# Kernel optimization log

Hardware: AMD Instinct MI355X
Metric: run time of the kernel (lower is better)

The kernel has to match this reference:

```python
import jax, jax.numpy as jnp
import numpy as np

B, C, H, W = 2, 256, 64, 64
NUM_HEADS = 4
HEAD_DIM = C // NUM_HEADS
N = H * W


def setup_inputs() -> dict:
    key = jax.random.key(0)
    ks = jax.random.split(key, 10)
    x = jax.random.normal(ks[0], (B, C, H, W), dtype=jnp.float32)
    # mostly-True mask; diagonal forced True so every row has a valid key
    m = jax.random.uniform(ks[1], (B, N, N)) > 0.1
    spatial_mask = m | jnp.eye(N, dtype=bool)[None]
    s = 1.0 / np.sqrt(C)
    wq = jax.random.normal(ks[2], (C, C), dtype=jnp.float32) * s
    bq = jnp.zeros((C,), jnp.float32)
    wk = jax.random.normal(ks[3], (C, C), dtype=jnp.float32) * s
    bk = jnp.zeros((C,), jnp.float32)
    wv = jax.random.normal(ks[4], (C, C), dtype=jnp.float32) * s
    bv = jnp.zeros((C,), jnp.float32)
    # torch zero-inits out_proj; use random weights for a non-trivial baseline
    wo = jax.random.normal(ks[5], (C, C), dtype=jnp.float32) * s
    bo = jnp.zeros((C,), jnp.float32)
    return {"x": x, "spatial_mask": spatial_mask, "wq": wq, "bq": bq,
            "wk": wk, "bk": bk, "wv": wv, "bv": bv, "wo": wo, "bo": bo}


def reference(x, spatial_mask, wq, bq, wk, bk, wv, bv, wo, bo):
    b, c, h, w = x.shape
    n = h * w
    nh, hd = NUM_HEADS, HEAD_DIM
    scale = hd ** -0.5
    x_flat = x.reshape(b, c, n).transpose(0, 2, 1)           # [b, n, c]
    q = (x_flat @ wq.T + bq).reshape(b, n, nh, hd).transpose(0, 2, 1, 3)
    k = (x_flat @ wk.T + bk).reshape(b, n, nh, hd).transpose(0, 2, 1, 3)
    v = (x_flat @ wv.T + bv).reshape(b, n, nh, hd).transpose(0, 2, 1, 3)
    logits = jnp.einsum('bhqd,bhkd->bhqk', q, k) * scale      # [b, nh, n, n]
    logits = jnp.where(spatial_mask[:, None], logits, -jnp.inf)
    attn = jax.nn.softmax(logits, axis=-1)                    # dropout = identity (eval)
    out = jnp.einsum('bhqk,bhkd->bhqd', attn, v)              # [b, nh, n, hd]
    out = out.transpose(0, 2, 1, 3).reshape(b, n, c)
    out = out @ wo.T + bo
    return out.transpose(0, 2, 1).reshape(b, c, h, w)
```

## Files before the change

kernel.cpp:

```cpp
#include <hip/hip_runtime.h>
#include <math.h>

namespace {
constexpr int B_    = 2;
constexpr int C_    = 256;
constexpr int NHEAD = 4;
constexpr int HDIM  = 64;
constexpr int NTOK  = 4096;
constexpr float SCALE = 0.125f;
constexpr float LOG2E = 1.44269504f;
}

typedef _Float16 half8  __attribute__((ext_vector_type(8)));
typedef _Float16 half4  __attribute__((ext_vector_type(4)));
typedef __fp16   fp16x2 __attribute__((ext_vector_type(2)));
typedef float    floatx4 __attribute__((ext_vector_type(4)));

__global__ __launch_bounds__(256) void pack_mask(
    const unsigned int* __restrict__ m32, unsigned int* __restrict__ packed)
{
    int c0 = 0, c1 = 0, c2 = 0, c3 = 0;
    #pragma unroll
    for (int i = 0; i < 16; i++) {
        const unsigned int d = m32[i];
        c0 += (d == 0x00000001u);
        c1 += (d == 0x3F803F80u);
        c2 += (d == 0x3F800000u);
        c3 += (d == 0x01010101u);
    }
    int fmt = 1, best = c1;
    if (c0 > best) { best = c0; fmt = 0; }
    if (c2 > best) { best = c2; fmt = 2; }
    if (c3 > best) { best = c3; fmt = 3; }

    const unsigned int W = blockIdx.x * 256 + threadIdx.x;
    unsigned int bits = 0;
    if (fmt == 1) {
        const uint4* p4 = (const uint4*)(m32 + (size_t)W * 16);
        #pragma unroll
        for (int i = 0; i < 4; i++) {
            const uint4 v = p4[i];
            const unsigned int d[4] = { v.x, v.y, v.z, v.w };
            #pragma unroll
            for (int j = 0; j < 4; j++) {
                const int e = i * 8 + j * 2;
                bits |= ((d[j] & 0xFFFFu) ? 1u : 0u) << e;
                bits |= ((d[j] >> 16)     ? 1u : 0u) << (e + 1);
            }
        }
    } else if (fmt != 3) {
        const uint4* p4 = (const uint4*)(m32 + (size_t)W * 32);
        #pragma unroll
        for (int i = 0; i < 8; i++) {
            const uint4 v = p4[i];
            bits |= (v.x ? 1u : 0u) << (i * 4 + 0);
            bits |= (v.y ? 1u : 0u) << (i * 4 + 1);
            bits |= (v.z ? 1u : 0u) << (i * 4 + 2);
            bits |= (v.w ? 1u : 0u) << (i * 4 + 3);
        }
    } else {
        const uint4* p4 = (const uint4*)(m32 + (size_t)W * 8);
        #pragma unroll
        for (int i = 0; i < 2; i++) {
            const uint4 v = p4[i];
            const unsigned int d[4] = { v.x, v.y, v.z, v.w };
            #pragma unroll
            for (int j = 0; j < 4; j++) {
                const int e = (i * 4 + j) * 4;
                bits |= ((d[j] & 0x000000FFu) ? 1u : 0u) << (e + 0);
                bits |= ((d[j] & 0x0000FF00u) ? 1u : 0u) << (e + 1);
                bits |= ((d[j] & 0x00FF0000u) ? 1u : 0u) << (e + 2);
                bits |= ((d[j] & 0xFF000000u) ? 1u : 0u) << (e + 3);
            }
        }
    }
    packed[W] = bits;
}

__global__ __launch_bounds__(256) void qkv_mfma(
    const float* __restrict__ x,
    const float* __restrict__ wq, const float* __restrict__ bq,
    const float* __restrict__ wk, const float* __restrict__ bk,
    const float* __restrict__ wv, const float* __restrict__ bv,
    _Float16* __restrict__ qo, _Float16* __restrict__ ko,
    _Float16* __restrict__ vo)
{
    const int nt = blockIdx.x;
    const int b  = blockIdx.y;
    const int p  = blockIdx.z;

    const float* w; const float* bias;
    if (p == 0)      { w = wq; bias = bq; }
    else if (p == 1) { w = wk; bias = bk; }
    else             { w = wv; bias = bv; }

    const int t    = threadIdx.x;
    const int wid  = t >> 6;
    const int lane = t & 63;
    const int quad = lane >> 4;
    const int l15  = lane & 15;
    const int n0   = nt * 64;

    __shared__ _Float16 xsh[64 * 264];
    __shared__ _Float16 wsh[64 * 72];
    __shared__ _Float16 tbuf[64 * 72];

    const int srow = t >> 2;
    const int sc   = (t & 3) * 16;

    {
        const int cr = t >> 4;
        const int nu = (t & 15) * 4;
        const float* xb = x + (size_t)b * C_ * NTOK;
        #pragma unroll
        for (int cc = 0; cc < 16; cc++) {
            const int cl = cc * 16 + cr;
            const float4 v = *(const float4*)&xb[(size_t)cl * NTOK + n0 + nu];
            xsh[(nu + 0) * 264 + cl] = (_Float16)v.x;
            xsh[(nu + 1) * 264 + cl] = (_Float16)v.y;
            xsh[(nu + 2) * 264 + cl] = (_Float16)v.z;
            xsh[(nu + 3) * 264 + cl] = (_Float16)v.w;
        }
    }

    for (int h = 0; h < NHEAD; h++) {
        const int co0 = h * 64;
        floatx4 acc[4];
        #pragma unroll
        for (int i = 0; i < 4; i++) acc[i] = (floatx4)0.f;

        for (int c0 = 0; c0 < C_; c0 += 64) {
            {
                const float* wr = &w[(size_t)(co0 + srow) * C_ + c0 + sc];
                half8 h0, h1;
                #pragma unroll
                for (int u = 0; u < 2; u++) {
                    const float4 a = *(const float4*)&wr[u * 4];
                    h0[u*4+0]=(_Float16)a.x; h0[u*4+1]=(_Float16)a.y;
                    h0[u*4+2]=(_Float16)a.z; h0[u*4+3]=(_Float16)a.w;
                }
                #pragma unroll
                for (int u = 0; u < 2; u++) {
                    const float4 a = *(const float4*)&wr[8 + u * 4];
                    h1[u*4+0]=(_Float16)a.x; h1[u*4+1]=(_Float16)a.y;
                    h1[u*4+2]=(_Float16)a.z; h1[u*4+3]=(_Float16)a.w;
                }
                *(half8*)&wsh[srow * 72 + sc]     = h0;
                *(half8*)&wsh[srow * 72 + sc + 8] = h1;
            }
            __syncthreads();
            const half8 a0 = *(const half8*)&wsh[(wid * 16 + l15) * 72 + quad * 8];
            const half8 a1 = *(const half8*)&wsh[(wid * 16 + l15) * 72 + 32 + quad * 8];
            #pragma unroll
            for (int nt2 = 0; nt2 < 4; nt2++) {
                const half8 b0 = *(const half8*)&xsh[(nt2 * 16 + l15) * 264 + c0 + quad * 8];
                const half8 b1 = *(const half8*)&xsh[(nt2 * 16 + l15) * 264 + c0 + 32 + quad * 8];
                acc[nt2] = __builtin_amdgcn_mfma_f32_16x16x32_f16(a0, b0, acc[nt2], 0, 0, 0);
                acc[nt2] = __builtin_amdgcn_mfma_f32_16x16x32_f16(a1, b1, acc[nt2], 0, 0, 0);
            }
            __syncthreads();
        }

        const float4 bb4 = *(const float4*)&bias[co0 + wid * 16 + quad * 4];
        const float bb[4] = { bb4.x, bb4.y, bb4.z, bb4.w };

        if (p < 2) {
            const float osc = (p == 0) ? (SCALE * LOG2E) : 1.0f;
            #pragma unroll
            for (int nt2 = 0; nt2 < 4; nt2++) {
                half4 hv;
                #pragma unroll
                for (int i = 0; i < 4; i++)
                    hv[i] = (_Float16)((acc[nt2][i] + bb[i]) * osc);
                *(half4*)&tbuf[(nt2 * 16 + l15) * 72 + wid * 16 + quad * 4] = hv;
            }
            __syncthreads();
            _Float16* dh = (p == 0 ? qo : ko) + (size_t)(b * NHEAD + h) * NTOK * HDIM;
            const half8 o0 = *(const half8*)&tbuf[srow * 72 + sc];
            const half8 o1 = *(const half8*)&tbuf[srow * 72 + sc + 8];
            *(half8*)&dh[(size_t)(n0 + srow) * HDIM + sc]     = o0;
            *(half8*)&dh[(size_t)(n0 + srow) * HDIM + sc + 8] = o1;
        } else {
            #pragma unroll
            for (int nt2 = 0; nt2 < 4; nt2++)
                #pragma unroll
                for (int i = 0; i < 4; i++)
                    tbuf[(wid * 16 + quad * 4 + i) * 72 + nt2 * 16 + l15] =
                        (_Float16)(acc[nt2][i] + bb[i]);
            __syncthreads();
            _Float16* vth = vo + (size_t)(b * NHEAD + h) * HDIM * NTOK;
            const half8 o0 = *(const half8*)&tbuf[srow * 72 + sc];
            const half8 o1 = *(const half8*)&tbuf[srow * 72 + sc + 8];
            *(half8*)&vth[(size_t)srow * NTOK + n0 + sc]     = o0;
            *(half8*)&vth[(size_t)srow * NTOK + n0 + sc + 8] = o1;
        }
        __syncthreads();
    }
}

__global__ __launch_bounds__(512) void attn(
    const _Float16* __restrict__ q, const _Float16* __restrict__ k,
    const _Float16* __restrict__ vt, const unsigned int* __restrict__ mpacked,
    _Float16* __restrict__ ao)
{
    const int b  = blockIdx.z;
    const int h  = blockIdx.y;
    const int q0 = blockIdx.x * 64;
    const int t    = threadIdx.x;
    const int w    = t >> 6;
    const int lane = t & 63;
    const int quad = lane >> 4;
    const int l15  = lane & 15;
    const int half = w >> 2;
    const int w4   = w & 3;
    const int koff = half * (NTOK / 2);

    __shared__ __align__(16) _Float16 ksA[64 * 72];
    __shared__ __align__(16) _Float16 vsA[64 * 72];
    __shared__ __align__(16) _Float16 psA[64 * 72];
    __shared__ __align__(16) _Float16 ksB[64 * 72];
    __shared__ __align__(16) _Float16 vsB[64 * 72];
    __shared__ __align__(16) _Float16 psB[64 * 72];

    _Float16* ksc = half ? ksB : ksA;
    _Float16* vsc = half ? vsB : vsA;
    _Float16* ps  = half ? psB : psA;

    const size_t head_off = (size_t)(b * NHEAD + h) * NTOK * HDIM;
    const _Float16* qb  = q  + head_off;
    const _Float16* kb  = k  + head_off;
    const _Float16* vtb = vt + head_off;
    const unsigned int* mrow = mpacked + (size_t)b * NTOK * 128;

    const int qrow = q0 + w4 * 16 + l15;
    half8 aq0 = *(const half8*)&qb[(size_t)qrow * HDIM + quad * 8];
    half8 aq1 = *(const half8*)&qb[(size_t)qrow * HDIM + 32 + quad * 8];
    const unsigned int* mq = &mrow[(size_t)qrow * 128];

    const int tl   = t & 255;
    const int srow = tl >> 2;
    const int scol = (tl & 3) * 16;

    half8 kreg0 = *(const half8*)&kb[(size_t)(koff + srow) * HDIM + scol];
    half8 kreg1 = *(const half8*)&kb[(size_t)(koff + srow) * HDIM + scol + 8];
    half8 vreg0 = *(const half8*)&vtb[(size_t)srow * NTOK + koff + scol];
    half8 vreg1 = *(const half8*)&vtb[(size_t)srow * NTOK + koff + scol + 8];

    float l_loc = 0.f;
    floatx4 o_acc[4];
    #pragma unroll
    for (int i = 0; i < 4; i++) o_acc[i] = (floatx4)0.f;

    _Float16* psrow = &ps[(w4 * 16 + l15) * 72];

    for (int kt = 0; kt < NTOK / 128; kt++) {
        const int k0 = koff + kt * 64;
        __syncthreads();
        *(half8*)&ksc[srow * 72 + scol]     = kreg0;
        *(half8*)&ksc[srow * 72 + scol + 8] = kreg1;
        *(half8*)&vsc[srow * 72 + scol]     = vreg0;
        *(half8*)&vsc[srow * 72 + scol + 8] = vreg1;
        __syncthreads();

        if (kt + 1 < NTOK / 128) {
            kreg0 = *(const half8*)&kb[(size_t)(k0 + 64 + srow) * HDIM + scol];
            kreg1 = *(const half8*)&kb[(size_t)(k0 + 64 + srow) * HDIM + scol + 8];
            vreg0 = *(const half8*)&vtb[(size_t)srow * NTOK + k0 + 64 + scol];
            vreg1 = *(const half8*)&vtb[(size_t)srow * NTOK + k0 + 64 + scol + 8];
        }
        const uint2 mw = *(const uint2*)&mq[k0 >> 5];

        floatx4 sa[4];
        #pragma unroll
        for (int ct = 0; ct < 4; ct++) {
            sa[ct] = (floatx4)0.f;
            const half8 ka0 = *(const half8*)&ksc[(ct * 16 + l15) * 72 + quad * 8];
            const half8 ka1 = *(const half8*)&ksc[(ct * 16 + l15) * 72 + 32 + quad * 8];
            sa[ct] = __builtin_amdgcn_mfma_f32_16x16x32_f16(ka0, aq0, sa[ct], 0, 0, 0);
            sa[ct] = __builtin_amdgcn_mfma_f32_16x16x32_f16(ka1, aq1, sa[ct], 0, 0, 0);
        }

        #pragma unroll
        for (int ct = 0; ct < 4; ct++) {
            const unsigned int word = (ct < 2) ? mw.x : mw.y;
            const unsigned nib = (word >> (((ct & 1) << 4) + quad * 4)) & 0xFu;
            const float p0 = __builtin_amdgcn_exp2f((nib & 1u) ? sa[ct][0] : -3.0e38f);
            const float p1 = __builtin_amdgcn_exp2f((nib & 2u) ? sa[ct][1] : -3.0e38f);
            const float p2 = __builtin_amdgcn_exp2f((nib & 4u) ? sa[ct][2] : -3.0e38f);
            const float p3 = __builtin_amdgcn_exp2f((nib & 8u) ? sa[ct][3] : -3.0e38f);
            l_loc += (p0 + p1) + (p2 + p3);
            const fp16x2 lo = __builtin_amdgcn_cvt_pkrtz(p0, p1);
            const fp16x2 hi = __builtin_amdgcn_cvt_pkrtz(p2, p3);
            half4 pv;
            pv[0] = (_Float16)lo[0]; pv[1] = (_Float16)lo[1];
            pv[2] = (_Float16)hi[0]; pv[3] = (_Float16)hi[1];
            *(half4*)&psrow[ct * 16 + quad * 4] = pv;
        }

        const half8 pb0 = *(const half8*)&psrow[quad * 8];
        const half8 pb1 = *(const half8*)&psrow[32 + quad * 8];
        #pragma unroll
        for (int dt = 0; dt < 4; dt++) {
            const half8 va0 = *(const half8*)&vsc[(dt * 16 + l15) * 72 + quad * 8];
            const half8 va1 = *(const half8*)&vsc[(dt * 16 + l15) * 72 + 32 + quad * 8];
            o_acc[dt] = __builtin_amdgcn_mfma_f32_16x16x32_f16(va0, pb0, o_acc[dt], 0, 0, 0);
            o_acc[dt] = __builtin_amdgcn_mfma_f32_16x16x32_f16(va1, pb1, o_acc[dt], 0, 0, 0);
        }
    }

    l_loc += __shfl_xor(l_loc, 16, 64);
    l_loc += __shfl_xor(l_loc, 32, 64);

    __syncthreads();
    float* oex = (float*)ksA;
    float* lex = (float*)vsA;
    if (w >= 4) {
        float* dst = &oex[((size_t)(w - 4) * 64 + lane) * 16];
        #pragma unroll
        for (int dt = 0; dt < 4; dt++)
            *(floatx4*)&dst[dt * 4] = o_acc[dt];
        if (quad == 0) lex[(w - 4) * 16 + l15] = l_loc;
    }
    __syncthreads();
    if (w < 4) {
        const float* src = &oex[((size_t)w * 64 + lane) * 16];
        const float lt = l_loc + lex[w * 16 + l15];
        const float inv = (lt > 0.f) ? (1.0f / lt) : 0.f;
        _Float16* aob = ao + ((size_t)b * NTOK + q0 + w * 16 + l15) * C_ + h * 64;
        #pragma unroll
        for (int dt = 0; dt < 4; dt++) {
            const floatx4 o2 = *(const floatx4*)&src[dt * 4];
            half4 r;
            #pragma unroll
            for (int rr = 0; rr < 4; rr++)
                r[rr] = (_Float16)((o_acc[dt][rr] + o2[rr]) * inv);
            *(half4*)&aob[dt * 16 + quad * 4] = r;
        }
    }
}

__global__ __launch_bounds__(256) void out_mfma(
    const _Float16* __restrict__ ao, const float* __restrict__ wo,
    const float* __restrict__ bo, float* __restrict__ out)
{
    const int nt  = blockIdx.x;
    const int cot = blockIdx.y;
    const int b   = blockIdx.z;
    const int t    = threadIdx.x;
    const int wid  = t >> 6;
    const int lane = t & 63;
    const int quad = lane >> 4;
    const int l15  = lane & 15;
    const int n0  = nt * 64;
    const int co0 = cot * 64;

    __shared__ _Float16 wsh[64 * 72];
    __shared__ _Float16 ash[64 * 72];
    __shared__ float    tf[64 * 68];

    const int srow = t >> 2;
    const int sc   = (t & 3) * 16;

    floatx4 acc[4];
    #pragma unroll
    for (int i = 0; i < 4; i++) acc[i] = (floatx4)0.f;

    const _Float16* aob = ao + ((size_t)b * NTOK + n0) * C_;

    for (int c0 = 0; c0 < C_; c0 += 64) {
        {
            const float* wr = &wo[(size_t)(co0 + srow) * C_ + c0 + sc];
            half8 h0, h1;
            #pragma unroll
            for (int u = 0; u < 2; u++) {
                const float4 a = *(const float4*)&wr[u * 4];
                h0[u*4+0]=(_Float16)a.x; h0[u*4+1]=(_Float16)a.y;
                h0[u*4+2]=(_Float16)a.z; h0[u*4+3]=(_Float16)a.w;
            }
            #pragma unroll
            for (int u = 0; u < 2; u++) {
                const float4 a = *(const float4*)&wr[8 + u * 4];
                h1[u*4+0]=(_Float16)a.x; h1[u*4+1]=(_Float16)a.y;
                h1[u*4+2]=(_Float16)a.z; h1[u*4+3]=(_Float16)a.w;
            }
            *(half8*)&wsh[srow * 72 + sc]     = h0;
            *(half8*)&wsh[srow * 72 + sc + 8] = h1;
        }
        {
            const _Float16* ar = &aob[(size_t)srow * C_ + c0 + sc];
            *(half8*)&ash[srow * 72 + sc]     = *(const half8*)&ar[0];
            *(half8*)&ash[srow * 72 + sc + 8] = *(const half8*)&ar[8];
        }
        __syncthreads();
        const half8 a0 = *(const half8*)&wsh[(wid * 16 + l15) * 72 + quad * 8];
        const half8 a1 = *(const half8*)&wsh[(wid * 16 + l15) * 72 + 32 + quad * 8];
        #pragma unroll
        for (int nt2 = 0; nt2 < 4; nt2++) {
            const half8 b0 = *(const half8*)&ash[(nt2 * 16 + l15) * 72 + quad * 8];
            const half8 b1 = *(const half8*)&ash[(nt2 * 16 + l15) * 72 + 32 + quad * 8];
            acc[nt2] = __builtin_amdgcn_mfma_f32_16x16x32_f16(a0, b0, acc[nt2], 0, 0, 0);
            acc[nt2] = __builtin_amdgcn_mfma_f32_16x16x32_f16(a1, b1, acc[nt2], 0, 0, 0);
        }
        __syncthreads();
    }

    #pragma unroll
    for (int nt2 = 0; nt2 < 4; nt2++)
        #pragma unroll
        for (int i = 0; i < 4; i++)
            tf[(wid * 16 + quad * 4 + i) * 68 + nt2 * 16 + l15] = acc[nt2][i];
    __syncthreads();

    const int row = t >> 2;
    const int c4  = (t & 3) * 16;
    const float bb = bo[co0 + row];
    float* orow = &out[((size_t)(b * C_ + co0 + row)) * NTOK + n0 + c4];
    #pragma unroll
    for (int u = 0; u < 4; u++) {
        float4 v = *(const float4*)&tf[row * 68 + c4 + u * 4];
        v.x += bb; v.y += bb; v.z += bb; v.w += bb;
        *(float4*)&orow[u * 4] = v;
    }
}

extern "C" void kernel_launch(void* const* d_in, const int* in_sizes, int n_in,
                              void* d_out, int out_size, void* d_ws, size_t ws_size,
                              hipStream_t stream) {
    const float* x    = (const float*)d_in[0];
    const void*  mask = d_in[1];
    const float* wq   = (const float*)d_in[2];
    const float* bq   = (const float*)d_in[3];
    const float* wk   = (const float*)d_in[4];
    const float* bk   = (const float*)d_in[5];
    const float* wv   = (const float*)d_in[6];
    const float* bv   = (const float*)d_in[7];
    const float* wo   = (const float*)d_in[8];
    const float* bo   = (const float*)d_in[9];
    float* out = (float*)d_out;

    const size_t qkv_elems = (size_t)B_ * NHEAD * NTOK * HDIM;
    _Float16* wsh = (_Float16*)d_ws;
    _Float16* qbuf  = wsh;
    _Float16* kbuf  = wsh + qkv_elems;
    _Float16* vtbuf = wsh + 2 * qkv_elems;
    _Float16* aobuf = wsh + 3 * qkv_elems;
    unsigned int* mpacked = (unsigned int*)(wsh + 4 * qkv_elems);

    pack_mask<<<dim3((B_ * NTOK * 128) / 256), 256, 0, stream>>>(
        (const unsigned int*)mask, mpacked);
    qkv_mfma<<<dim3(NTOK / 64, B_, 3), 256, 0, stream>>>(
        x, wq, bq, wk, bk, wv, bv, qbuf, kbuf, vtbuf);
    attn<<<dim3(NTOK / 64, NHEAD, B_), 512, 0, stream>>>(
        qbuf, kbuf, vtbuf, mpacked, aobuf);
    out_mfma<<<dim3(NTOK / 64, C_ / 64, B_), 256, 0, stream>>>(
        aobuf, wo, bo, out);
}
```

Baseline: 309.3 us.

## Split attention over four key ranges, merge partials in out-projection, fuse mask packing

The attention kernel now uses 256-thread blocks, each handling one quarter of the keys, with four times as many blocks. Unnormalized fp16 partial outputs and row sums are written to workspace. The output-projection kernel sums the four partials and normalizes them while staging its A tile. Mask packing moves into extra blocks of the QKV kernel, which removes one launch. The cost is four times the intermediate output traffic, partial sums accumulated in fp16, and the P tile now reusing the K shared buffer, which needs an extra barrier.

```diff
diff --git a/kernel.cpp b/kernel.cpp
--- a/kernel.cpp
+++ b/kernel.cpp
@@ -9,73 +9,13 @@
 constexpr int NTOK  = 4096;
 constexpr float SCALE = 0.125f;
 constexpr float LOG2E = 1.44269504f;
+constexpr int NSPLIT = 4;
 }
 
 typedef _Float16 half8  __attribute__((ext_vector_type(8)));
 typedef _Float16 half4  __attribute__((ext_vector_type(4)));
 typedef __fp16   fp16x2 __attribute__((ext_vector_type(2)));
 typedef float    floatx4 __attribute__((ext_vector_type(4)));
-
-__global__ __launch_bounds__(256) void pack_mask(
-    const unsigned int* __restrict__ m32, unsigned int* __restrict__ packed)
-{
-    int c0 = 0, c1 = 0, c2 = 0, c3 = 0;
-    #pragma unroll
-    for (int i = 0; i < 16; i++) {
-        const unsigned int d = m32[i];
-        c0 += (d == 0x00000001u);
-        c1 += (d == 0x3F803F80u);
-        c2 += (d == 0x3F800000u);
-        c3 += (d == 0x01010101u);
-    }
-    int fmt = 1, best = c1;
-    if (c0 > best) { best = c0; fmt = 0; }
-    if (c2 > best) { best = c2; fmt = 2; }
-    if (c3 > best) { best = c3; fmt = 3; }
-
-    const unsigned int W = blockIdx.x * 256 + threadIdx.x;
-    unsigned int bits = 0;
-    if (fmt == 1) {
-        const uint4* p4 = (const uint4*)(m32 + (size_t)W * 16);
-        #pragma unroll
-        for (int i = 0; i < 4; i++) {
-            const uint4 v = p4[i];
-            const unsigned int d[4] = { v.x, v.y, v.z, v.w };
-            #pragma unroll
-            for (int j = 0; j < 4; j++) {
-                const int e = i * 8 + j * 2;
-                bits |= ((d[j] & 0xFFFFu) ? 1u : 0u) << e;
-                bits |= ((d[j] >> 16)     ? 1u : 0u) << (e + 1);
-            }
-        }
-    } else if (fmt != 3) {
-        const uint4* p4 = (const uint4*)(m32 + (size_t)W * 32);
-        #pragma unroll
-        for (int i = 0; i < 8; i++) {
-            const uint4 v = p4[i];
-            bits |= (v.x ? 1u : 0u) << (i * 4 + 0);
-            bits |= (v.y ? 1u : 0u) << (i * 4 + 1);
-            bits |= (v.z ? 1u : 0u) << (i * 4 + 2);
-            bits |= (v.w ? 1u : 0u) << (i * 4 + 3);
-        }
-    } else {
-        const uint4* p4 = (const uint4*)(m32 + (size_t)W * 8);
-        #pragma unroll
-        for (int i = 0; i < 2; i++) {
-            const uint4 v = p4[i];
-            const unsigned int d[4] = { v.x, v.y, v.z, v.w };
-            #pragma unroll
-            for (int j = 0; j < 4; j++) {
-                const int e = (i * 4 + j) * 4;
-                bits |= ((d[j] & 0x000000FFu) ? 1u : 0u) << (e + 0);
-                bits |= ((d[j] & 0x0000FF00u) ? 1u : 0u) << (e + 1);
-                bits |= ((d[j] & 0x00FF0000u) ? 1u : 0u) << (e + 2);
-                bits |= ((d[j] & 0xFF000000u) ? 1u : 0u) << (e + 3);
-            }
-        }
-    }
-    packed[W] = bits;
-}
 
 __global__ __launch_bounds__(256) void qkv_mfma(
     const float* __restrict__ x,
@@ -83,18 +23,83 @@
     const float* __restrict__ wk, const float* __restrict__ bk,
     const float* __restrict__ wv, const float* __restrict__ bv,
     _Float16* __restrict__ qo, _Float16* __restrict__ ko,
-    _Float16* __restrict__ vo)
+    _Float16* __restrict__ vo,
+    const unsigned int* __restrict__ m32, unsigned int* __restrict__ packed)
 {
+    const int p = blockIdx.z;
+    const int t = threadIdx.x;
+
+    if (p == 3) {
+        int c0 = 0, c1 = 0, c2 = 0, c3 = 0;
+        #pragma unroll
+        for (int i = 0; i < 16; i++) {
+            const unsigned int d = m32[i];
+            c0 += (d == 0x00000001u);
+            c1 += (d == 0x3F803F80u);
+            c2 += (d == 0x3F800000u);
+            c3 += (d == 0x01010101u);
+        }
+        int fmt = 1, best = c1;
+        if (c0 > best) { best = c0; fmt = 0; }
+        if (c2 > best) { best = c2; fmt = 2; }
+        if (c3 > best) { best = c3; fmt = 3; }
+
+        const unsigned int pblk = blockIdx.y * 64 + blockIdx.x;
+        for (int it = 0; it < 32; it++) {
+            const unsigned int W = pblk * 8192 + it * 256 + t;
+            unsigned int bits = 0;
+            if (fmt == 1) {
+                const uint4* p4 = (const uint4*)(m32 + (size_t)W * 16);
+                #pragma unroll
+                for (int i = 0; i < 4; i++) {
+                    const uint4 v = p4[i];
+                    const unsigned int d[4] = { v.x, v.y, v.z, v.w };
+                    #pragma unroll
+                    for (int j = 0; j < 4; j++) {
+                        const int e = i * 8 + j * 2;
+                        bits |= ((d[j] & 0xFFFFu) ? 1u : 0u) << e;
+                        bits |= ((d[j] >> 16)     ? 1u : 0u) << (e + 1);
+                    }
+                }
+            } else if (fmt != 3) {
+                const uint4* p4 = (const uint4*)(m32 + (size_t)W * 32);
+                #pragma unroll
+                for (int i = 0; i < 8; i++) {
+                    const uint4 v = p4[i];
+                    bits |= (v.x ? 1u : 0u) << (i * 4 + 0);
+                    bits |= (v.y ? 1u : 0u) << (i * 4 + 1);
+                    bits |= (v.z ? 1u : 0u) << (i * 4 + 2);
+                    bits |= (v.w ? 1u : 0u) << (i * 4 + 3);
+                }
+            } else {
+                const uint4* p4 = (const uint4*)(m32 + (size_t)W * 8);
+                #pragma unroll
+                for (int i = 0; i < 2; i++) {
+                    const uint4 v = p4[i];
+                    const unsigned int d[4] = { v.x, v.y, v.z, v.w };
+                    #pragma unroll
+                    for (int j = 0; j < 4; j++) {
+                        const int e = (i * 4 + j) * 4;
+                        bits |= ((d[j] & 0x000000FFu) ? 1u : 0u) << (e + 0);
+                        bits |= ((d[j] & 0x0000FF00u) ? 1u : 0u) << (e + 1);
+                        bits |= ((d[j] & 0x00FF0000u) ? 1u : 0u) << (e + 2);
+                        bits |= ((d[j] & 0xFF000000u) ? 1u : 0u) << (e + 3);
+                    }
+                }
+            }
+            packed[W] = bits;
+        }
+        return;
+    }
+
     const int nt = blockIdx.x;
     const int b  = blockIdx.y;
-    const int p  = blockIdx.z;
 
     const float* w; const float* bias;
     if (p == 0)      { w = wq; bias = bq; }
     else if (p == 1) { w = wk; bias = bk; }
     else             { w = wv; bias = bv; }
 
-    const int t    = threadIdx.x;
     const int wid  = t >> 6;
     const int lane = t & 63;
     const int quad = lane >> 4;
@@ -198,33 +203,24 @@
     }
 }
 
-__global__ __launch_bounds__(512) void attn(
+__global__ __launch_bounds__(256, 8) void attn(
     const _Float16* __restrict__ q, const _Float16* __restrict__ k,
     const _Float16* __restrict__ vt, const unsigned int* __restrict__ mpacked,
-    _Float16* __restrict__ ao)
+    _Float16* __restrict__ aoP, float* __restrict__ lP)
 {
-    const int b  = blockIdx.z;
+    const int b  = blockIdx.z >> 2;
+    const int s  = blockIdx.z & 3;
     const int h  = blockIdx.y;
     const int q0 = blockIdx.x * 64;
     const int t    = threadIdx.x;
-    const int w    = t >> 6;
+    const int w4   = t >> 6;
     const int lane = t & 63;
     const int quad = lane >> 4;
     const int l15  = lane & 15;
-    const int half = w >> 2;
-    const int w4   = w & 3;
-    const int koff = half * (NTOK / 2);
-
-    __shared__ __align__(16) _Float16 ksA[64 * 72];
-    __shared__ __align__(16) _Float16 vsA[64 * 72];
-    __shared__ __align__(16) _Float16 psA[64 * 72];
-    __shared__ __align__(16) _Float16 ksB[64 * 72];
-    __shared__ __align__(16) _Float16 vsB[64 * 72];
-    __shared__ __align__(16) _Float16 psB[64 * 72];
-
-    _Float16* ksc = half ? ksB : ksA;
-    _Float16* vsc = half ? vsB : vsA;
-    _Float16* ps  = half ? psB : psA;
+    const int koff = s * (NTOK / NSPLIT);
+
+    __shared__ __align__(16) _Float16 ks[64 * 72];
+    __shared__ __align__(16) _Float16 vs[64 * 72];
 
     const size_t head_off = (size_t)(b * NHEAD + h) * NTOK * HDIM;
     const _Float16* qb  = q  + head_off;
@@ -237,9 +233,8 @@
     half8 aq1 = *(const half8*)&qb[(size_t)qrow * HDIM + 32 + quad * 8];
     const unsigned int* mq = &mrow[(size_t)qrow * 128];
 
-    const int tl   = t & 255;
-    const int srow = tl >> 2;
-    const int scol = (tl & 3) * 16;
+    const int srow = t >> 2;
+    const int scol = (t & 3) * 16;
 
     half8 kreg0 = *(const half8*)&kb[(size_t)(koff + srow) * HDIM + scol];
     half8 kreg1 = *(const half8*)&kb[(size_t)(koff + srow) * HDIM + scol + 8];
@@ -251,18 +246,18 @@
     #pragma unroll
     for (int i = 0; i < 4; i++) o_acc[i] = (floatx4)0.f;
 
-    _Float16* psrow = &ps[(w4 * 16 + l15) * 72];
-
-    for (int kt = 0; kt < NTOK / 128; kt++) {
+    _Float16* psrow = &ks[(w4 * 16 + l15) * 72];
+
+    for (int kt = 0; kt < NTOK / (64 * NSPLIT); kt++) {
         const int k0 = koff + kt * 64;
         __syncthreads();
-        *(half8*)&ksc[srow * 72 + scol]     = kreg0;
-        *(half8*)&ksc[srow * 72 + scol + 8] = kreg1;
-        *(half8*)&vsc[srow * 72 + scol]     = vreg0;
-        *(half8*)&vsc[srow * 72 + scol + 8] = vreg1;
-        __syncthreads();
-
-        if (kt + 1 < NTOK / 128) {
+        *(half8*)&ks[srow * 72 + scol]     = kreg0;
+        *(half8*)&ks[srow * 72 + scol + 8] = kreg1;
+        *(half8*)&vs[srow * 72 + scol]     = vreg0;
+        *(half8*)&vs[srow * 72 + scol + 8] = vreg1;
+        __syncthreads();
+
+        if (kt + 1 < NTOK / (64 * NSPLIT)) {
             kreg0 = *(const half8*)&kb[(size_t)(k0 + 64 + srow) * HDIM + scol];
             kreg1 = *(const half8*)&kb[(size_t)(k0 + 64 + srow) * HDIM + scol + 8];
             vreg0 = *(const half8*)&vtb[(size_t)srow * NTOK + k0 + 64 + scol];
@@ -274,11 +269,12 @@
         #pragma unroll
         for (int ct = 0; ct < 4; ct++) {
             sa[ct] = (floatx4)0.f;
-            const half8 ka0 = *(const half8*)&ksc[(ct * 16 + l15) * 72 + quad * 8];
-            const half8 ka1 = *(const half8*)&ksc[(ct * 16 + l15) * 72 + 32 + quad * 8];
+            const half8 ka0 = *(const half8*)&ks[(ct * 16 + l15) * 72 + quad * 8];
+            const half8 ka1 = *(const half8*)&ks[(ct * 16 + l15) * 72 + 32 + quad * 8];
             sa[ct] = __builtin_amdgcn_mfma_f32_16x16x32_f16(ka0, aq0, sa[ct], 0, 0, 0);
             sa[ct] = __builtin_amdgcn_mfma_f32_16x16x32_f16(ka1, aq1, sa[ct], 0, 0, 0);
         }
+        __syncthreads();
 
         #pragma unroll
         for (int ct = 0; ct < 4; ct++) {
@@ -301,8 +297,8 @@
         const half8 pb1 = *(const half8*)&psrow[32 + quad * 8];
         #pragma unroll
         for (int dt = 0; dt < 4; dt++) {
-            const half8 va0 = *(const half8*)&vsc[(dt * 16 + l15) * 72 + quad * 8];
-            const half8 va1 = *(const half8*)&vsc[(dt * 16 + l15) * 72 + 32 + quad * 8];
+            const half8 va0 = *(const half8*)&vs[(dt * 16 + l15) * 72 + quad * 8];
+            const half8 va1 = *(const half8*)&vs[(dt * 16 + l15) * 72 + 32 + quad * 8];
             o_acc[dt] = __builtin_amdgcn_mfma_f32_16x16x32_f16(va0, pb0, o_acc[dt], 0, 0, 0);
             o_acc[dt] = __builtin_amdgcn_mfma_f32_16x16x32_f16(va1, pb1, o_acc[dt], 0, 0, 0);
         }
@@ -311,37 +307,22 @@
     l_loc += __shfl_xor(l_loc, 16, 64);
     l_loc += __shfl_xor(l_loc, 32, 64);
 
-    __syncthreads();
-    float* oex = (float*)ksA;
-    float* lex = (float*)vsA;
-    if (w >= 4) {
-        float* dst = &oex[((size_t)(w - 4) * 64 + lane) * 16];
-        #pragma unroll
-        for (int dt = 0; dt < 4; dt++)
-            *(floatx4*)&dst[dt * 4] = o_acc[dt];
-        if (quad == 0) lex[(w - 4) * 16 + l15] = l_loc;
-    }
-    __syncthreads();
-    if (w < 4) {
-        const float* src = &oex[((size_t)w * 64 + lane) * 16];
-        const float lt = l_loc + lex[w * 16 + l15];
-        const float inv = (lt > 0.f) ? (1.0f / lt) : 0.f;
-        _Float16* aob = ao + ((size_t)b * NTOK + q0 + w * 16 + l15) * C_ + h * 64;
-        #pragma unroll
-        for (int dt = 0; dt < 4; dt++) {
-            const floatx4 o2 = *(const floatx4*)&src[dt * 4];
-            half4 r;
-            #pragma unroll
-            for (int rr = 0; rr < 4; rr++)
-                r[rr] = (_Float16)((o_acc[dt][rr] + o2[rr]) * inv);
-            *(half4*)&aob[dt * 16 + quad * 4] = r;
-        }
-    }
+    _Float16* aob = aoP + (((size_t)s * B_ + b) * NTOK + q0 + w4 * 16 + l15) * C_ + h * 64;
+    #pragma unroll
+    for (int dt = 0; dt < 4; dt++) {
+        half4 r;
+        #pragma unroll
+        for (int rr = 0; rr < 4; rr++) r[rr] = (_Float16)o_acc[dt][rr];
+        *(half4*)&aob[dt * 16 + quad * 4] = r;
+    }
+    if (quad == 0)
+        lP[(((size_t)s * B_ + b) * NHEAD + h) * NTOK + q0 + w4 * 16 + l15] = l_loc;
 }
 
 __global__ __launch_bounds__(256) void out_mfma(
-    const _Float16* __restrict__ ao, const float* __restrict__ wo,
-    const float* __restrict__ bo, float* __restrict__ out)
+    const _Float16* __restrict__ aoP, const float* __restrict__ lP,
+    const float* __restrict__ wo, const float* __restrict__ bo,
+    float* __restrict__ out)
 {
     const int nt  = blockIdx.x;
     const int cot = blockIdx.y;
@@ -357,15 +338,27 @@
     __shared__ _Float16 wsh[64 * 72];
     __shared__ _Float16 ash[64 * 72];
     __shared__ float    tf[64 * 68];
+    __shared__ float    linv[4][64];
 
     const int srow = t >> 2;
     const int sc   = (t & 3) * 16;
+
+    {
+        const int hh  = t >> 6;
+        const int tok = t & 63;
+        float sum = 0.f;
+        #pragma unroll
+        for (int s = 0; s < 4; s++)
+            sum += lP[(((size_t)s * B_ + b) * NHEAD + hh) * NTOK + n0 + tok];
+        linv[hh][tok] = (sum > 0.f) ? (1.0f / sum) : 0.f;
+    }
+    __syncthreads();
 
     floatx4 acc[4];
     #pragma unroll
     for (int i = 0; i < 4; i++) acc[i] = (floatx4)0.f;
 
-    const _Float16* aob = ao + ((size_t)b * NTOK + n0) * C_;
+    const size_t sstride = (size_t)B_ * NTOK * C_;
 
     for (int c0 = 0; c0 < C_; c0 += 64) {
         {
@@ -387,9 +380,17 @@
             *(half8*)&wsh[srow * 72 + sc + 8] = h1;
         }
         {
-            const _Float16* ar = &aob[(size_t)srow * C_ + c0 + sc];
-            *(half8*)&ash[srow * 72 + sc]     = *(const half8*)&ar[0];
-            *(half8*)&ash[srow * 72 + sc + 8] = *(const half8*)&ar[8];
+            const _Float16 il = (_Float16)linv[c0 >> 6][srow];
+            const _Float16* ar = aoP + ((size_t)b * NTOK + n0 + srow) * C_ + c0 + sc;
+            half8 s0 = *(const half8*)&ar[0];
+            half8 s1 = *(const half8*)&ar[8];
+            #pragma unroll
+            for (int s = 1; s < 4; s++) {
+                s0 += *(const half8*)&ar[s * sstride];
+                s1 += *(const half8*)&ar[s * sstride + 8];
+            }
+            *(half8*)&ash[srow * 72 + sc]     = s0 * il;
+            *(half8*)&ash[srow * 72 + sc + 8] = s1 * il;
         }
         __syncthreads();
         const half8 a0 = *(const half8*)&wsh[(wid * 16 + l15) * 72 + quad * 8];
@@ -443,15 +444,16 @@
     _Float16* qbuf  = wsh;
     _Float16* kbuf  = wsh + qkv_elems;
     _Float16* vtbuf = wsh + 2 * qkv_elems;
-    _Float16* aobuf = wsh + 3 * qkv_elems;
-    unsigned int* mpacked = (unsigned int*)(wsh + 4 * qkv_elems);
-
-    pack_mask<<<dim3((B_ * NTOK * 128) / 256), 256, 0, stream>>>(
+    _Float16* aoP   = wsh + 3 * qkv_elems;
+    float* lP = (float*)(wsh + 7 * qkv_elems);
+    unsigned int* mpacked =
+        (unsigned int*)(lP + (size_t)NSPLIT * B_ * NHEAD * NTOK);
+
+    qkv_mfma<<<dim3(NTOK / 64, B_, 4), 256, 0, stream>>>(
+        x, wq, bq, wk, bk, wv, bv, qbuf, kbuf, vtbuf,
         (const unsigned int*)mask, mpacked);
-    qkv_mfma<<<dim3(NTOK / 64, B_, 3), 256, 0, stream>>>(
-        x, wq, bq, wk, bk, wv, bv, qbuf, kbuf, vtbuf);
-    attn<<<dim3(NTOK / 64, NHEAD, B_), 512, 0, stream>>>(
-        qbuf, kbuf, vtbuf, mpacked, aobuf);
+    attn<<<dim3(NTOK / 64, NHEAD, B_ * NSPLIT), 256, 0, stream>>>(
+        qbuf, kbuf, vtbuf, mpacked, aoP, lP);
     out_mfma<<<dim3(NTOK / 64, C_ / 64, B_), 256, 0, stream>>>(
-        aobuf, wo, bo, out);
+        aoP, lP, wo, bo, out);
 }
```

New measurement: 427.1 us. 38.1% more time.

## Fuse mask packing into QKV launch and alias P tile onto K smem

Applied to the files above, without the earlier changes.

Removes the separate pack_mask kernel and runs mask packing on an extra z-slice of the QKV projection grid, where 128 blocks each pack 8192 words in a loop. The attention kernel drops its dedicated P buffers and writes P over the K tile, adding a barrier after the QK MFMAs so that overwrite is safe. It also sets a min-blocks hint on launch bounds. The aim is to cut one launch and reduce shared memory for higher occupancy, at the cost of an extra barrier per iteration and a less parallel packing phase.

```diff
diff --git a/kernel.cpp b/kernel.cpp
--- a/kernel.cpp
+++ b/kernel.cpp
@@ -16,85 +16,89 @@
 typedef __fp16   fp16x2 __attribute__((ext_vector_type(2)));
 typedef float    floatx4 __attribute__((ext_vector_type(4)));
 
-__global__ __launch_bounds__(256) void pack_mask(
-    const unsigned int* __restrict__ m32, unsigned int* __restrict__ packed)
-{
-    int c0 = 0, c1 = 0, c2 = 0, c3 = 0;
-    #pragma unroll
-    for (int i = 0; i < 16; i++) {
-        const unsigned int d = m32[i];
-        c0 += (d == 0x00000001u);
-        c1 += (d == 0x3F803F80u);
-        c2 += (d == 0x3F800000u);
-        c3 += (d == 0x01010101u);
-    }
-    int fmt = 1, best = c1;
-    if (c0 > best) { best = c0; fmt = 0; }
-    if (c2 > best) { best = c2; fmt = 2; }
-    if (c3 > best) { best = c3; fmt = 3; }
-
-    const unsigned int W = blockIdx.x * 256 + threadIdx.x;
-    unsigned int bits = 0;
-    if (fmt == 1) {
-        const uint4* p4 = (const uint4*)(m32 + (size_t)W * 16);
-        #pragma unroll
-        for (int i = 0; i < 4; i++) {
-            const uint4 v = p4[i];
-            const unsigned int d[4] = { v.x, v.y, v.z, v.w };
-            #pragma unroll
-            for (int j = 0; j < 4; j++) {
-                const int e = i * 8 + j * 2;
-                bits |= ((d[j] & 0xFFFFu) ? 1u : 0u) << e;
-                bits |= ((d[j] >> 16)     ? 1u : 0u) << (e + 1);
-            }
-        }
-    } else if (fmt != 3) {
-        const uint4* p4 = (const uint4*)(m32 + (size_t)W * 32);
-        #pragma unroll
-        for (int i = 0; i < 8; i++) {
-            const uint4 v = p4[i];
-            bits |= (v.x ? 1u : 0u) << (i * 4 + 0);
-            bits |= (v.y ? 1u : 0u) << (i * 4 + 1);
-            bits |= (v.z ? 1u : 0u) << (i * 4 + 2);
-            bits |= (v.w ? 1u : 0u) << (i * 4 + 3);
-        }
-    } else {
-        const uint4* p4 = (const uint4*)(m32 + (size_t)W * 8);
-        #pragma unroll
-        for (int i = 0; i < 2; i++) {
-            const uint4 v = p4[i];
-            const unsigned int d[4] = { v.x, v.y, v.z, v.w };
-            #pragma unroll
-            for (int j = 0; j < 4; j++) {
-                const int e = (i * 4 + j) * 4;
-                bits |= ((d[j] & 0x000000FFu) ? 1u : 0u) << (e + 0);
-                bits |= ((d[j] & 0x0000FF00u) ? 1u : 0u) << (e + 1);
-                bits |= ((d[j] & 0x00FF0000u) ? 1u : 0u) << (e + 2);
-                bits |= ((d[j] & 0xFF000000u) ? 1u : 0u) << (e + 3);
-            }
-        }
-    }
-    packed[W] = bits;
-}
-
 __global__ __launch_bounds__(256) void qkv_mfma(
     const float* __restrict__ x,
     const float* __restrict__ wq, const float* __restrict__ bq,
     const float* __restrict__ wk, const float* __restrict__ bk,
     const float* __restrict__ wv, const float* __restrict__ bv,
     _Float16* __restrict__ qo, _Float16* __restrict__ ko,
-    _Float16* __restrict__ vo)
+    _Float16* __restrict__ vo,
+    const unsigned int* __restrict__ m32, unsigned int* __restrict__ packed)
 {
+    const int p = blockIdx.z;
+    const int t = threadIdx.x;
+
+    if (p == 3) {
+        int c0 = 0, c1 = 0, c2 = 0, c3 = 0;
+        #pragma unroll
+        for (int i = 0; i < 16; i++) {
+            const unsigned int d = m32[i];
+            c0 += (d == 0x00000001u);
+            c1 += (d == 0x3F803F80u);
+            c2 += (d == 0x3F800000u);
+            c3 += (d == 0x01010101u);
+        }
+        int fmt = 1, best = c1;
+        if (c0 > best) { best = c0; fmt = 0; }
+        if (c2 > best) { best = c2; fmt = 2; }
+        if (c3 > best) { best = c3; fmt = 3; }
+
+        const unsigned int pblk = blockIdx.y * 64 + blockIdx.x;
+        for (int it = 0; it < 32; it++) {
+            const unsigned int W = pblk * 8192 + it * 256 + t;
+            unsigned int bits = 0;
+            if (fmt == 1) {
+                const uint4* p4 = (const uint4*)(m32 + (size_t)W * 16);
+                #pragma unroll
+                for (int i = 0; i < 4; i++) {
+                    const uint4 v = p4[i];
+                    const unsigned int d[4] = { v.x, v.y, v.z, v.w };
+                    #pragma unroll
+                    for (int j = 0; j < 4; j++) {
+                        const int e = i * 8 + j * 2;
+                        bits |= ((d[j] & 0xFFFFu) ? 1u : 0u) << e;
+                        bits |= ((d[j] >> 16)     ? 1u : 0u) << (e + 1);
+                    }
+                }
+            } else if (fmt != 3) {
+                const uint4* p4 = (const uint4*)(m32 + (size_t)W * 32);
+                #pragma unroll
+                for (int i = 0; i < 8; i++) {
+                    const uint4 v = p4[i];
+                    bits |= (v.x ? 1u : 0u) << (i * 4 + 0);
+                    bits |= (v.y ? 1u : 0u) << (i * 4 + 1);
+                    bits |= (v.z ? 1u : 0u) << (i * 4 + 2);
+                    bits |= (v.w ? 1u : 0u) << (i * 4 + 3);
+                }
+            } else {
+                const uint4* p4 = (const uint4*)(m32 + (size_t)W * 8);
+                #pragma unroll
+                for (int i = 0; i < 2; i++) {
+                    const uint4 v = p4[i];
+                    const unsigned int d[4] = { v.x, v.y, v.z, v.w };
+                    #pragma unroll
+                    for (int j = 0; j < 4; j++) {
+                        const int e = (i * 4 + j) * 4;
+                        bits |= ((d[j] & 0x000000FFu) ? 1u : 0u) << (e + 0);
+                        bits |= ((d[j] & 0x0000FF00u) ? 1u : 0u) << (e + 1);
+                        bits |= ((d[j] & 0x00FF0000u) ? 1u : 0u) << (e + 2);
+                        bits |= ((d[j] & 0xFF000000u) ? 1u : 0u) << (e + 3);
+                    }
+                }
+            }
+            packed[W] = bits;
+        }
+        return;
+    }
+
     const int nt = blockIdx.x;
     const int b  = blockIdx.y;
-    const int p  = blockIdx.z;
 
     const float* w; const float* bias;
     if (p == 0)      { w = wq; bias = bq; }
     else if (p == 1) { w = wk; bias = bk; }
     else             { w = wv; bias = bv; }
 
-    const int t    = threadIdx.x;
     const int wid  = t >> 6;
     const int lane = t & 63;
     const int quad = lane >> 4;
@@ -198,7 +202,7 @@
     }
 }
 
-__global__ __launch_bounds__(512) void attn(
+__global__ __launch_bounds__(512, 8) void attn(
     const _Float16* __restrict__ q, const _Float16* __restrict__ k,
     const _Float16* __restrict__ vt, const unsigned int* __restrict__ mpacked,
     _Float16* __restrict__ ao)
@@ -215,16 +219,9 @@
     const int w4   = w & 3;
     const int koff = half * (NTOK / 2);
 
-    __shared__ __align__(16) _Float16 ksA[64 * 72];
-    __shared__ __align__(16) _Float16 vsA[64 * 72];
-    __shared__ __align__(16) _Float16 psA[64 * 72];
-    __shared__ __align__(16) _Float16 ksB[64 * 72];
-    __shared__ __align__(16) _Float16 vsB[64 * 72];
-    __shared__ __align__(16) _Float16 psB[64 * 72];
-
-    _Float16* ksc = half ? ksB : ksA;
-    _Float16* vsc = half ? vsB : vsA;
-    _Float16* ps  = half ? psB : psA;
+    __shared__ __align__(16) _Float16 smem[4 * 4608];
+    _Float16* ksc = smem + (size_t)half * 9216;
+    _Float16* vsc = ksc + 4608;
 
     const size_t head_off = (size_t)(b * NHEAD + h) * NTOK * HDIM;
     const _Float16* qb  = q  + head_off;
@@ -251,7 +248,7 @@
     #pragma unroll
     for (int i = 0; i < 4; i++) o_acc[i] = (floatx4)0.f;
 
-    _Float16* psrow = &ps[(w4 * 16 + l15) * 72];
+    _Float16* psrow = &ksc[(w4 * 16 + l15) * 72];
 
     for (int kt = 0; kt < NTOK / 128; kt++) {
         const int k0 = koff + kt * 64;
@@ -279,6 +276,7 @@
             sa[ct] = __builtin_amdgcn_mfma_f32_16x16x32_f16(ka0, aq0, sa[ct], 0, 0, 0);
             sa[ct] = __builtin_amdgcn_mfma_f32_16x16x32_f16(ka1, aq1, sa[ct], 0, 0, 0);
         }
+        __syncthreads();
 
         #pragma unroll
         for (int ct = 0; ct < 4; ct++) {
@@ -312,8 +310,8 @@
     l_loc += __shfl_xor(l_loc, 32, 64);
 
     __syncthreads();
-    float* oex = (float*)ksA;
-    float* lex = (float*)vsA;
+    float* oex = (float*)smem;
+    float* lex = (float*)(smem + 12288);
     if (w >= 4) {
         float* dst = &oex[((size_t)(w - 4) * 64 + lane) * 16];
         #pragma unroll
@@ -446,10 +444,9 @@
     _Float16* aobuf = wsh + 3 * qkv_elems;
     unsigned int* mpacked = (unsigned int*)(wsh + 4 * qkv_elems);
 
-    pack_mask<<<dim3((B_ * NTOK * 128) / 256), 256, 0, stream>>>(
+    qkv_mfma<<<dim3(NTOK / 64, B_, 4), 256, 0, stream>>>(
+        x, wq, bq, wk, bk, wv, bv, qbuf, kbuf, vtbuf,
         (const unsigned int*)mask, mpacked);
-    qkv_mfma<<<dim3(NTOK / 64, B_, 3), 256, 0, stream>>>(
-        x, wq, bq, wk, bk, wv, bv, qbuf, kbuf, vtbuf);
     attn<<<dim3(NTOK / 64, NHEAD, B_), 512, 0, stream>>>(
         qbuf, kbuf, vtbuf, mpacked, aobuf);
     out_mfma<<<dim3(NTOK / 64, C_ / 64, B_), 256, 0, stream>>>(
```

After: 457.9 us. 48.1% more time.
